# Kernel optimization log

Hardware: AMD Instinct MI355X
Metric: run time of the kernel (lower is better)

## Reference

```python
import jax, jax.numpy as jnp
import numpy as np
from jax import lax

L, H, NUM_CONVS, KSIZE = 8192, 128, 4, 7
EPS = 1e-5


def _pos_encoding(length, dim, dtype):
    pos = jnp.arange(length, dtype=jnp.float32)[:, None]
    i = jnp.arange(dim, dtype=jnp.float32)[None, :]
    angle = pos / jnp.power(10000.0, (2.0 * jnp.floor(i / 2.0)) / dim)
    pe = jnp.where((jnp.arange(dim) % 2 == 0)[None, :], jnp.sin(angle), jnp.cos(angle))
    return pe.astype(dtype)


def _layer_norm(x):
    mu = jnp.mean(x, axis=-1, keepdims=True)
    var = jnp.mean(jnp.square(x - mu), axis=-1, keepdims=True)
    return (x - mu) * lax.rsqrt(var + EPS)


def _conv1d_same(x, w, b):
    # x: [L, H]; w: [H_out, H_in, K]; b: [H_out]. SAME padding over sequence.
    lhs = x.T[None]  # [1, H, L]
    out = lax.conv_general_dilated(lhs, w, window_strides=(1,), padding='SAME',
                                   dimension_numbers=('NCH', 'OIH', 'NCH'))
    return (out[0] + b[:, None]).T  # [L, H]


def setup_inputs() -> dict:
    key = jax.random.key(0)
    ks = jax.random.split(key, 12)
    s = 0.02
    return {
        'x': jax.random.normal(ks[0], (L, H), jnp.float32),
        'conv_w': jax.random.normal(ks[1], (NUM_CONVS, H, H, KSIZE), jnp.float32) * s,
        'conv_b': jax.random.normal(ks[2], (NUM_CONVS, H), jnp.float32) * s,
        'Wq': jax.random.normal(ks[3], (H, H), jnp.float32) * s,
        'bq': jax.random.normal(ks[4], (H,), jnp.float32) * s,
        'Wk': jax.random.normal(ks[5], (H, H), jnp.float32) * s,
        'bk': jax.random.normal(ks[6], (H,), jnp.float32) * s,
        'Wv': jax.random.normal(ks[7], (H, H), jnp.float32) * s,
        'bv': jax.random.normal(ks[8], (H,), jnp.float32) * s,
        'Wff': jax.random.normal(ks[9], (H, H), jnp.float32) * s,
        'bff': jax.random.normal(ks[10], (H,), jnp.float32) * s,
    }


def reference(x, conv_w, conv_b, Wq, bq, Wk, bk, Wv, bv, Wff, bff):
    h = x + _pos_encoding(x.shape[0], x.shape[1], x.dtype)
    # conv stack: LN -> conv -> residual, repeated num_convs times
    for i in range(NUM_CONVS):
        residual = h
        h = _conv1d_same(_layer_norm(h), conv_w[i], conv_b[i]) + residual
    # self-attention (single-head as written in the source)
    residual = h
    n = _layer_norm(h)
    q = n @ Wq.T + bq
    k = n @ Wk.T + bk
    v = n @ Wv.T + bv
    scale = 1.0 / jnp.sqrt(jnp.asarray(H, h.dtype))
    attn = jax.nn.softmax((q @ k.T) * scale, axis=-1)  # [L, L]
    h = attn @ v + residual
    # feed-forward
    residual = h
    h = jax.nn.relu(_layer_norm(h) @ Wff.T + bff) + residual
    return h
```

## Files before the change

### kernel.cpp

```cpp
#include <hip/hip_runtime.h>

#define LL 8192
#define HH 128

typedef __attribute__((ext_vector_type(8))) short short8v;
typedef __attribute__((ext_vector_type(4))) short short4v;
typedef __attribute__((ext_vector_type(4))) float f32x4;
typedef __attribute__((ext_vector_type(16))) float f32x16;

__device__ inline short f2bf(float f) {
    union { float f; unsigned u; } x; x.f = f;
    unsigned r = (x.u + 0x7fffu + ((x.u >> 16) & 1u)) >> 16;
    return (short)r;
}
__device__ inline float bf2f(short s) {
    union { unsigned u; float f; } x; x.u = ((unsigned)(unsigned short)s) << 16;
    return x.f;
}

__device__ inline float fexp2(float x) {
#if defined(__has_builtin)
#if __has_builtin(__builtin_amdgcn_exp2f)
    return __builtin_amdgcn_exp2f(x);
#else
    return __expf(x * 0.6931471805599453f);
#endif
#else
    return __expf(x * 0.6931471805599453f);
#endif
}

__device__ inline unsigned pack_hi16(unsigned hi, unsigned lo) {
#if defined(__has_builtin)
#if __has_builtin(__builtin_amdgcn_perm)
    return __builtin_amdgcn_perm(hi, lo, 0x07060302u);
#endif
#endif
    return (lo >> 16) | (hi & 0xffff0000u);
}

__device__ inline void plane32swap(unsigned& a, unsigned& b) {
#if defined(__has_builtin)
#if __has_builtin(__builtin_amdgcn_permlane32_swap)
    typedef unsigned u2v __attribute__((ext_vector_type(2)));
    u2v r = __builtin_amdgcn_permlane32_swap(a, b, false, false);
    a = r[0]; b = r[1];
    return;
#endif
#endif
    asm volatile("v_permlane32_swap_b32 %0, %1" : "+v"(a), "+v"(b));
}

__device__ inline short* sAp(short* base, int row, int col) {
    int byte = (row << 8) + (col << 1);
    byte ^= (row & 7) << 4;
    return (short*)((char*)base + byte);
}

__device__ inline short8v ln_pack8(const float* rowF, int l15) {
    const float4 a = *(const float4*)&rowF[l15 * 8];
    const float4 b = *(const float4*)&rowF[l15 * 8 + 4];
    float s  = (a.x + a.y) + (a.z + a.w) + (b.x + b.y) + (b.z + b.w);
    float s2 = a.x * a.x + a.y * a.y + a.z * a.z + a.w * a.w
             + b.x * b.x + b.y * b.y + b.z * b.z + b.w * b.w;
#pragma unroll
    for (int off = 1; off <= 8; off <<= 1) {
        s  += __shfl_xor(s,  off, 64);
        s2 += __shfl_xor(s2, off, 64);
    }
    float mu = s * (1.f / 128.f);
    float var = s2 * (1.f / 128.f) - mu * mu;
    float rstd = rsqrtf(var + 1e-5f);
    short8v r;
    r[0] = f2bf((a.x - mu) * rstd);
    r[1] = f2bf((a.y - mu) * rstd);
    r[2] = f2bf((a.z - mu) * rstd);
    r[3] = f2bf((a.w - mu) * rstd);
    r[4] = f2bf((b.x - mu) * rstd);
    r[5] = f2bf((b.y - mu) * rstd);
    r[6] = f2bf((b.z - mu) * rstd);
    r[7] = f2bf((b.w - mu) * rstd);
    return r;
}

__global__ __launch_bounds__(256) void repack_all(const float* __restrict__ x,
                                                  const float* __restrict__ w,
                                                  const float* __restrict__ Wq,
                                                  const float* __restrict__ Wk,
                                                  const float* __restrict__ Wv,
                                                  const float* __restrict__ bq,
                                                  const float* __restrict__ bk,
                                                  const float* __restrict__ bv,
                                                  const float* __restrict__ Wff,
                                                  short* __restrict__ wkb,
                                                  short* __restrict__ wqkvb,
                                                  float* __restrict__ b3,
                                                  short* __restrict__ wffb,
                                                  float* __restrict__ h0) {
    const float qs = 0.08838834764831845f * 1.4426950408889634f;
    int idx = blockIdx.x * 256 + threadIdx.x;
    if (idx < 458752) {
        int k = idx % 7;
        int t = idx / 7;
        int i = t % HH; t /= HH;
        int o = t % HH;
        int lay = t / HH;
        wkb[((lay * 7 + k) * HH + o) * HH + i] = f2bf(w[idx]);
    } else {
        int j = idx - 458752;
        if (j < 49152) {
            int t = j >> 14, r = j & 16383;
            float v = (t == 0) ? Wq[r] * qs : (t == 1) ? Wk[r] : Wv[r];
            wqkvb[j] = f2bf(v);
        } else if (j < 49536) {
            int jj = j - 49152;
            b3[jj] = (jj < 128) ? bq[jj] * qs : (jj < 256) ? bk[jj - 128] : bv[jj - 256];
        } else if (j < 65920) {
            int jj = j - 49536;
            wffb[jj] = f2bf(Wff[jj]);
        } else {
            int p = j - 65920;
            if (p < 262144) {
                int g = p >> 5, c4 = (p & 31) << 2;
                float4 val = *(const float4*)&x[g * HH + c4];
                float fg = (float)g;
#pragma unroll
                for (int h = 0; h < 2; h++) {
                    int i0 = c4 + h * 2;
                    float e = (float)i0 / 128.f;
                    float rev = fg * fexp2(e * -13.287712379549449f - 2.651496129472319f);
                    rev -= floorf(rev);
                    float ang = rev * 6.283185307179586f;
                    ((float*)&val)[h * 2]     += __sinf(ang);
                    ((float*)&val)[h * 2 + 1] += __cosf(ang);
                }
                *(float4*)&h0[g * HH + c4] = val;
            }
        }
    }
}

__global__ __launch_bounds__(256, 2) void conv4_qkv_kernel(const float* __restrict__ h0,
                                                           const short* __restrict__ wkb,
                                                           const float* __restrict__ conv_b,
                                                           const short* __restrict__ wqkvb,
                                                           const float* __restrict__ b3,
                                                           float* __restrict__ hB,
                                                           short* __restrict__ qb,
                                                           short* __restrict__ kb,
                                                           short* __restrict__ vt) {
    __shared__ float sF[40][132];
    __shared__ short sA[54 * 128];
    __shared__ short sT[4][32][17];
    int tid = threadIdx.x;
    int w = tid >> 6, lane = tid & 63;
    int l15 = lane & 15, quad = lane >> 4;
    int wg = blockIdx.x;
    int m0 = ((wg & 7) * 64 + (wg >> 3)) * 16;
    int c0 = w * 32;

    for (int idx = tid; idx < 40 * 32; idx += 256) {
        int r = idx >> 5, c4 = (idx & 31) << 2;
        int g = m0 - 12 + r;
        float4 val = make_float4(0.f, 0.f, 0.f, 0.f);
        if (g >= 0 && g < LL) val = *(const float4*)&h0[g * HH + c4];
        *(float4*)&sF[r][c4] = val;
    }
    __syncthreads();
#pragma unroll
    for (int rr = 0; rr < 3; rr++) {
        int row = rr * 16 + w * 4 + quad;
        if (row < 40)
            *(short8v*)sAp(sA, row, l15 * 8) = ln_pack8(&sF[row][0], l15);
    }
    __syncthreads();

    const float* cb = conv_b;
#define CONV_TILE(wl, B, aca, acb)                                                  \
    {                                                                               \
        for (int k = 0; k < 7; k++) {                                               \
            const short* bw0 = (wl) + (k * HH + c0 + l15) * HH;                     \
            const short* bw1 = bw0 + 16 * HH;                                       \
            _Pragma("unroll")                                                       \
            for (int ks = 0; ks < 4; ks++) {                                        \
                short8v bf0 = *(const short8v*)&bw0[ks * 32 + quad * 8];            \
                short8v bf1 = *(const short8v*)&bw1[ks * 32 + quad * 8];            \
                short8v af = *(const short8v*)sAp(sA, (B) - 3 + l15 + k,            \
                                                  ks * 32 + quad * 8);              \
                aca = __builtin_amdgcn_mfma_f32_16x16x32_bf16(af, bf0, aca, 0, 0, 0); \
                acb = __builtin_amdgcn_mfma_f32_16x16x32_bf16(af, bf1, acb, 0, 0, 0); \
            }                                                                       \
        }                                                                           \
    }

    {
        const short* wl = wkb + 0 * 7 * HH * HH;
        f32x4 a0a = (f32x4)(0.f), a0b = (f32x4)(0.f);
        f32x4 a1a = (f32x4)(0.f), a1b = (f32x4)(0.f);
        f32x4 a2a = (f32x4)(0.f), a2b = (f32x4)(0.f);
        CONV_TILE(wl, 3,  a0a, a0b);
        CONV_TILE(wl, 19, a1a, a1b);
        CONV_TILE(wl, 35, a2a, a2b);
        float bl = cb[0 * HH + c0 + l15], bh = cb[0 * HH + c0 + 16 + l15];
#pragma unroll
        for (int r = 0; r < 4; r++) {
            int rr0 = quad * 4 + r;
            sF[3 + rr0][c0 + l15]       += a0a[r] + bl;
            sF[3 + rr0][c0 + 16 + l15]  += a0b[r] + bh;
            sF[19 + rr0][c0 + l15]      += a1a[r] + bl;
            sF[19 + rr0][c0 + 16 + l15] += a1b[r] + bh;
            if (rr0 < 2) {
                sF[35 + rr0][c0 + l15]      += a2a[r] + bl;
                sF[35 + rr0][c0 + 16 + l15] += a2b[r] + bh;
            }
        }
    }
    __syncthreads();
#pragma unroll
    for (int rr = 0; rr < 3; rr++) {
        int row = 3 + rr * 16 + w * 4 + quad;
        if (row < 37) {
            short8v pk = ln_pack8(&sF[row][0], l15);
            int g = m0 - 12 + row;
            if (g < 0 || g >= LL) pk = (short8v)(short)0;
            *(short8v*)sAp(sA, row, l15 * 8) = pk;
        }
    }
    __syncthreads();

    {
        const short* wl = wkb + 1 * 7 * HH * HH;
        f32x4 a0a = (f32x4)(0.f), a0b = (f32x4)(0.f);
        f32x4 a1a = (f32x4)(0.f), a1b = (f32x4)(0.f);
        CONV_TILE(wl, 6,  a0a, a0b);
        CONV_TILE(wl, 22, a1a, a1b);
        float bl = cb[1 * HH + c0 + l15], bh = cb[1 * HH + c0 + 16 + l15];
#pragma unroll
        for (int r = 0; r < 4; r++) {
            int rr0 = quad * 4 + r;
            sF[6 + rr0][c0 + l15]      += a0a[r] + bl;
            sF[6 + rr0][c0 + 16 + l15] += a0b[r] + bh;
            if (rr0 < 12) {
                sF[22 + rr0][c0 + l15]      += a1a[r] + bl;
                sF[22 + rr0][c0 + 16 + l15] += a1b[r] + bh;
            }
        }
    }
    __syncthreads();
#pragma unroll
    for (int rr = 0; rr < 2; rr++) {
        int row = 6 + rr * 16 + w * 4 + quad;
        if (row < 34) {
            short8v pk = ln_pack8(&sF[row][0], l15);
            int g = m0 - 12 + row;
            if (g < 0 || g >= LL) pk = (short8v)(short)0;
            *(short8v*)sAp(sA, row, l15 * 8) = pk;
        }
    }
    __syncthreads();

    {
        const short* wl = wkb + 2 * 7 * HH * HH;
        f32x4 a0a = (f32x4)(0.f), a0b = (f32x4)(0.f);
        f32x4 a1a = (f32x4)(0.f), a1b = (f32x4)(0.f);
        CONV_TILE(wl, 9,  a0a, a0b);
        CONV_TILE(wl, 25, a1a, a1b);
        float bl = cb[2 * HH + c0 + l15], bh = cb[2 * HH + c0 + 16 + l15];
#pragma unroll
        for (int r = 0; r < 4; r++) {
            int rr0 = quad * 4 + r;
            sF[9 + rr0][c0 + l15]      += a0a[r] + bl;
            sF[9 + rr0][c0 + 16 + l15] += a0b[r] + bh;
            if (rr0 < 6) {
                sF[25 + rr0][c0 + l15]      += a1a[r] + bl;
                sF[25 + rr0][c0 + 16 + l15] += a1b[r] + bh;
            }
        }
    }
    __syncthreads();
#pragma unroll
    for (int rr = 0; rr < 2; rr++) {
        int row = 9 + rr * 16 + w * 4 + quad;
        if (row < 31) {
            short8v pk = ln_pack8(&sF[row][0], l15);
            int g = m0 - 12 + row;
            if (g < 0 || g >= LL) pk = (short8v)(short)0;
            *(short8v*)sAp(sA, row, l15 * 8) = pk;
        }
    }
    __syncthreads();

    {
        const short* wl = wkb + 3 * 7 * HH * HH;
        f32x4 a0a = (f32x4)(0.f), a0b = (f32x4)(0.f);
        CONV_TILE(wl, 12, a0a, a0b);
        float bl = cb[3 * HH + c0 + l15], bh = cb[3 * HH + c0 + 16 + l15];
#pragma unroll
        for (int r = 0; r < 4; r++) {
            int rr0 = quad * 4 + r;
            int g = m0 + rr0;
            float v0 = sF[12 + rr0][c0 + l15]      + a0a[r] + bl;
            float v1 = sF[12 + rr0][c0 + 16 + l15] + a0b[r] + bh;
            sF[12 + rr0][c0 + l15]      = v0;
            sF[12 + rr0][c0 + 16 + l15] = v1;
            hB[g * HH + c0 + l15]      = v0;
            hB[g * HH + c0 + 16 + l15] = v1;
        }
    }
    __syncthreads();
#undef CONV_TILE
    {
        int row = w * 4 + quad;
        *(short8v*)sAp(sA, row, l15 * 8) = ln_pack8(&sF[12 + row][0], l15);
    }
    __syncthreads();
    short8v af4[4];
#pragma unroll
    for (int ks = 0; ks < 4; ks++)
        af4[ks] = *(const short8v*)sAp(sA, l15, ks * 32 + quad * 8);

    for (int t = 0; t < 3; t++) {
        f32x4 acc0 = (f32x4)(0.f), acc1 = (f32x4)(0.f);
        const short* b0 = wqkvb + (t * 128 + c0 + l15) * HH;
        const short* b1 = b0 + 16 * HH;
#pragma unroll
        for (int ks = 0; ks < 4; ks++) {
            short8v bf0 = *(const short8v*)&b0[ks * 32 + quad * 8];
            short8v bf1 = *(const short8v*)&b1[ks * 32 + quad * 8];
            acc0 = __builtin_amdgcn_mfma_f32_16x16x32_bf16(af4[ks], bf0, acc0, 0, 0, 0);
            acc1 = __builtin_amdgcn_mfma_f32_16x16x32_bf16(af4[ks], bf1, acc1, 0, 0, 0);
        }
        float qb0 = b3[t * 128 + c0 + l15], qb1 = b3[t * 128 + c0 + 16 + l15];
        if (t < 2) {
            short* o = (t == 0) ? qb : kb;
#pragma unroll
            for (int r = 0; r < 4; r++) {
                int lr = m0 + quad * 4 + r;
                o[lr * HH + c0 + l15]      = f2bf(acc0[r] + qb0);
                o[lr * HH + c0 + 16 + l15] = f2bf(acc1[r] + qb1);
            }
        } else {
#pragma unroll
            for (int r = 0; r < 4; r++) {
                sT[w][l15][quad * 4 + r]      = f2bf(acc0[r] + qb0);
                sT[w][16 + l15][quad * 4 + r] = f2bf(acc1[r] + qb1);
            }
            asm volatile("s_waitcnt lgkmcnt(0)" ::: "memory");
#pragma unroll
            for (int cc = 0; cc < 8; cc++) {
                int col = cc * 4 + quad;
                vt[(c0 + col) * LL + m0 + l15] = sT[w][col][l15];
            }
        }
    }
}

#define FBN 64
#define NSPLIT 8
#define SEGROWS (LL / NSPLIT)

__global__ __launch_bounds__(256, 2) void flash_mfma_kernel(const short* __restrict__ qs,
                                                            const short* __restrict__ ksrc,
                                                            const short* __restrict__ vsrc,
                                                            short* __restrict__ PO,
                                                            float* __restrict__ Pl) {
    __shared__ short sK[16 * 64 * 8];
    __shared__ short sV[16 * 64 * 8];

    const int tid = threadIdx.x;
    const int w = tid >> 6, lane = tid & 63;
    const int l31 = lane & 31, hi = lane >> 5;
    const int seg = blockIdx.x & 7;
    const int m0 = (blockIdx.x >> 3) * 128;
    const int jbeg = seg * SEGROWS;
    const int nchunk = SEGROWS >> 6;
    const int qrow = m0 + w * 32 + l31;

    short8v qf[8];
#pragma unroll
    for (int ks = 0; ks < 8; ks++)
        qf[ks] = *(const short8v*)&qs[qrow * HH + ks * 16 + hi * 8];

    float l_r = 0.f;
    f32x16 o_acc[4];
#pragma unroll
    for (int dt = 0; dt < 4; dt++) o_acc[dt] = (f32x16)(0.f);

    short8v kr[4], vr[4];
#pragma unroll
    for (int r = 0; r < 4; r++) {
        int s = w + 4 * r;
        kr[r] = *(const short8v*)&ksrc[(jbeg + (s >> 3) * 32 + l31) * HH + (s & 7) * 16 + hi * 8];
        vr[r] = *(const short8v*)&vsrc[((s >> 2) * 32 + l31) * LL + jbeg + (s & 3) * 16 + hi * 8];
    }

    for (int c = 0; c < nchunk; c++) {
        __syncthreads();
#pragma unroll
        for (int r = 0; r < 4; r++) {
            int s = w + 4 * r;
            *(short8v*)&sK[(s * 64 + lane) * 8] = kr[r];
            *(short8v*)&sV[(s * 64 + lane) * 8] = vr[r];
        }
        __syncthreads();
        if (c + 1 < nchunk) {
            const int j1 = jbeg + (c + 1) * FBN;
#pragma unroll
            for (int r = 0; r < 4; r++) {
                int s = w + 4 * r;
                kr[r] = *(const short8v*)&ksrc[(j1 + (s >> 3) * 32 + l31) * HH + (s & 7) * 16 + hi * 8];
                vr[r] = *(const short8v*)&vsrc[((s >> 2) * 32 + l31) * LL + j1 + (s & 3) * 16 + hi * 8];
            }
        }
        f32x16 s0 = (f32x16)(0.f), s1 = (f32x16)(0.f);
        __builtin_amdgcn_s_setprio(1);
#pragma unroll
        for (int ks = 0; ks < 8; ks++) {
            short8v kf0 = *(const short8v*)&sK[((ks) * 64 + lane) * 8];
            short8v kf1 = *(const short8v*)&sK[((8 + ks) * 64 + lane) * 8];
            s0 = __builtin_amdgcn_mfma_f32_32x32x16_bf16(kf0, qf[ks], s0, 0, 0, 0);
            s1 = __builtin_amdgcn_mfma_f32_32x32x16_bf16(kf1, qf[ks], s1, 0, 0, 0);
        }
        __builtin_amdgcn_s_setprio(0);
        short8v pfrag[4];
#pragma unroll
        for (int nt = 0; nt < 2; nt++) {
            const f32x16& sa = nt ? s1 : s0;
            unsigned pw[8];
#pragma unroll
            for (int m = 0; m < 8; m++) {
                float p0 = fexp2(sa[2 * m]);
                float p1 = fexp2(sa[2 * m + 1]);
                l_r += p0 + p1;
                union { float f; unsigned u; } u0, u1;
                u0.f = p0; u1.f = p1;
                pw[m] = pack_hi16(u1.u, u0.u);
            }
            plane32swap(pw[0], pw[2]);
            plane32swap(pw[1], pw[3]);
            plane32swap(pw[4], pw[6]);
            plane32swap(pw[5], pw[7]);
            union { unsigned u[4]; short8v v; } fa, fb;
            fa.u[0] = pw[0]; fa.u[1] = pw[1]; fa.u[2] = pw[2]; fa.u[3] = pw[3];
            fb.u[0] = pw[4]; fb.u[1] = pw[5]; fb.u[2] = pw[6]; fb.u[3] = pw[7];
            pfrag[nt * 2]     = fa.v;
            pfrag[nt * 2 + 1] = fb.v;
        }
        __builtin_amdgcn_s_setprio(1);
#pragma unroll
        for (int ks = 0; ks < 4; ks++)
#pragma unroll
            for (int dt = 0; dt < 4; dt++) {
                short8v vf = *(const short8v*)&sV[((dt * 4 + ks) * 64 + lane) * 8];
                o_acc[dt] = __builtin_amdgcn_mfma_f32_32x32x16_bf16(pfrag[ks], vf, o_acc[dt], 0, 0, 0);
            }
        __builtin_amdgcn_s_setprio(0);
    }
    float lsum = l_r + __shfl_xor(l_r, 32, 64);
    if (hi == 0)
        Pl[seg * LL + qrow] = lsum;
#pragma unroll
    for (int dt = 0; dt < 4; dt++)
#pragma unroll
        for (int i = 0; i < 16; i++) {
            int qr = (i & 3) + 8 * (i >> 2) + 4 * hi;
            PO[(size_t)seg * LL * HH + (size_t)(m0 + w * 32 + qr) * HH + dt * 32 + l31] =
                f2bf(o_acc[dt][i]);
        }
}

__global__ __launch_bounds__(256) void ff_kernel(const float* __restrict__ hin,
                                                 const short* __restrict__ PO,
                                                 const float* __restrict__ Pl,
                                                 const short* __restrict__ wffb,
                                                 const float* __restrict__ bff,
                                                 float* __restrict__ out) {
    __shared__ float sF[16][132];
    __shared__ short sA[16 * 128];
    __shared__ float sLi[16];
    int tid = threadIdx.x;
    int w = tid >> 6, lane = tid & 63;
    int l15 = lane & 15, quad = lane >> 4;
    int wg = blockIdx.x;
    int m0 = ((wg & 7) * 64 + (wg >> 3)) * 16;

    if (tid < 16) {
        float s = 0.f;
#pragma unroll
        for (int seg = 0; seg < NSPLIT; seg++) s += Pl[seg * LL + m0 + tid];
        sLi[tid] = 1.f / s;
    }
    __syncthreads();
    for (int idx = tid; idx < 16 * 32; idx += 256) {
        int r = idx >> 5, c4 = (idx & 31) << 2;
        float4 hv = *(const float4*)&hin[(m0 + r) * HH + c4];
        float s0 = 0.f, s1 = 0.f, s2 = 0.f, s3 = 0.f;
#pragma unroll
        for (int seg = 0; seg < NSPLIT; seg++) {
            short4v pv = *(const short4v*)&PO[(size_t)seg * LL * HH + (m0 + r) * HH + c4];
            s0 += bf2f(pv[0]); s1 += bf2f(pv[1]); s2 += bf2f(pv[2]); s3 += bf2f(pv[3]);
        }
        float li = sLi[r];
        *(float4*)&sF[r][c4] = make_float4(hv.x + s0 * li, hv.y + s1 * li,
                                           hv.z + s2 * li, hv.w + s3 * li);
    }
    __syncthreads();
    {
        int row = w * 4 + quad;
        *(short8v*)sAp(sA, row, l15 * 8) = ln_pack8(&sF[row][0], l15);
    }
    __syncthreads();
    int c0 = w * 32;
    f32x4 acc0 = (f32x4)(0.f), acc1 = (f32x4)(0.f);
    const short* b0 = wffb + (c0 + l15) * HH;
    const short* b1 = b0 + 16 * HH;
#pragma unroll
    for (int ks = 0; ks < 4; ks++) {
        short8v af = *(const short8v*)sAp(sA, l15, ks * 32 + quad * 8);
        short8v bf0 = *(const short8v*)&b0[ks * 32 + quad * 8];
        short8v bf1 = *(const short8v*)&b1[ks * 32 + quad * 8];
        acc0 = __builtin_amdgcn_mfma_f32_16x16x32_bf16(af, bf0, acc0, 0, 0, 0);
        acc1 = __builtin_amdgcn_mfma_f32_16x16x32_bf16(af, bf1, acc1, 0, 0, 0);
    }
    float bb0 = bff[c0 + l15], bb1 = bff[c0 + 16 + l15];
#pragma unroll
    for (int r = 0; r < 4; r++) {
        int lr = quad * 4 + r;
        out[(m0 + lr) * HH + c0 + l15]      = fmaxf(acc0[r] + bb0, 0.f) + sF[lr][c0 + l15];
        out[(m0 + lr) * HH + c0 + 16 + l15] = fmaxf(acc1[r] + bb1, 0.f) + sF[lr][c0 + 16 + l15];
    }
}

extern "C" void kernel_launch(void* const* d_in, const int* in_sizes, int n_in,
                              void* d_out, int out_size, void* d_ws, size_t ws_size,
                              hipStream_t stream) {
    const float* x      = (const float*)d_in[0];
    const float* conv_w = (const float*)d_in[1];
    const float* conv_b = (const float*)d_in[2];
    const float* Wq = (const float*)d_in[3];
    const float* bq = (const float*)d_in[4];
    const float* Wk = (const float*)d_in[5];
    const float* bk = (const float*)d_in[6];
    const float* Wv = (const float*)d_in[7];
    const float* bv = (const float*)d_in[8];
    const float* Wff = (const float*)d_in[9];
    const float* bff = (const float*)d_in[10];
    float* out = (float*)d_out;

    char* ws = (char*)d_ws;
    const size_t MB = 1u << 20;
    float* hB   = (float*)(ws);
    short* qb   = (short*)(ws + 4 * MB);
    short* kb   = (short*)(ws + 6 * MB);
    short* vt   = (short*)(ws + 8 * MB);
    float* Pl   = (float*)(ws + 10 * MB);
    short* wffb = (short*)(ws + 10 * MB + 524288);
    short* PO   = (short*)(ws + 10 * MB + 524288 + 32768);
    short* wkb   = (short*)(ws + 16 * MB);
    short* wqkvb = (short*)(ws + 17 * MB);
    float* b3    = (float*)(ws + 17 * MB + 131072);
    float* h0    = (float*)(ws + 18 * MB);

    repack_all<<<3074, 256, 0, stream>>>(x, conv_w, Wq, Wk, Wv, bq, bk, bv, Wff,
                                         wkb, wqkvb, b3, wffb, h0);
    conv4_qkv_kernel<<<LL / 16, 256, 0, stream>>>(h0, wkb, conv_b, wqkvb, b3,
                                                  hB, qb, kb, vt);
    flash_mfma_kernel<<<LL / 128 * NSPLIT, 256, 0, stream>>>(qb, kb, vt, PO, Pl);
    ff_kernel<<<LL / 16, 256, 0, stream>>>(hB, PO, Pl, wffb, bff, out);
}
```

Before: 195.0 us.

## Split conv/QKV kernel across eight waves with 16 output columns each

Doubles the conv4_qkv block size from 256 to 512 threads so each of eight waves owns 16 output columns instead of 32. Each wave's MFMA work is split across two accumulators by alternating k-slices, which keeps two independent dependency chains. Layer-norm packing is redone with a helper that stores two 4-element halves. The aim is more parallelism and latency hiding in the conv stage. The cost is extra per-wave LDS A-fragment reads, since A is now loaded per 16 columns, and heavier register pressure under launch bounds of 4 blocks of 512.

```diff
diff --git a/kernel.cpp b/kernel.cpp
--- a/kernel.cpp
+++ b/kernel.cpp
@@ -81,6 +81,30 @@
     r[6] = f2bf((b.z - mu) * rstd);
     r[7] = f2bf((b.w - mu) * rstd);
     return r;
+}
+
+__device__ inline void ln_store8(const float* rowF, int l15, short* sA, int row, bool zero) {
+    const float4 a = *(const float4*)&rowF[l15 * 4];
+    const float4 b = *(const float4*)&rowF[64 + l15 * 4];
+    float s  = (a.x + a.y) + (a.z + a.w) + (b.x + b.y) + (b.z + b.w);
+    float s2 = a.x * a.x + a.y * a.y + a.z * a.z + a.w * a.w
+             + b.x * b.x + b.y * b.y + b.z * b.z + b.w * b.w;
+#pragma unroll
+    for (int off = 1; off <= 8; off <<= 1) {
+        s  += __shfl_xor(s,  off, 64);
+        s2 += __shfl_xor(s2, off, 64);
+    }
+    float mu = s * (1.f / 128.f);
+    float var = s2 * (1.f / 128.f) - mu * mu;
+    float rstd = rsqrtf(var + 1e-5f);
+    short4v ra, rb;
+    ra[0] = f2bf((a.x - mu) * rstd); ra[1] = f2bf((a.y - mu) * rstd);
+    ra[2] = f2bf((a.z - mu) * rstd); ra[3] = f2bf((a.w - mu) * rstd);
+    rb[0] = f2bf((b.x - mu) * rstd); rb[1] = f2bf((b.y - mu) * rstd);
+    rb[2] = f2bf((b.z - mu) * rstd); rb[3] = f2bf((b.w - mu) * rstd);
+    if (zero) { ra = (short4v)(short)0; rb = (short4v)(short)0; }
+    *(short4v*)sAp(sA, row, l15 * 4)      = ra;
+    *(short4v*)sAp(sA, row, 64 + l15 * 4) = rb;
 }
 
 __global__ __launch_bounds__(256) void repack_all(const float* __restrict__ x,
@@ -140,7 +164,7 @@
     }
 }
 
-__global__ __launch_bounds__(256, 2) void conv4_qkv_kernel(const float* __restrict__ h0,
+__global__ __launch_bounds__(512, 4) void conv4_qkv_kernel(const float* __restrict__ h0,
                                                            const short* __restrict__ wkb,
                                                            const float* __restrict__ conv_b,
                                                            const short* __restrict__ wqkvb,
@@ -151,15 +175,15 @@
                                                            short* __restrict__ vt) {
     __shared__ float sF[40][132];
     __shared__ short sA[54 * 128];
-    __shared__ short sT[4][32][17];
+    __shared__ short sT[8][16][17];
     int tid = threadIdx.x;
     int w = tid >> 6, lane = tid & 63;
     int l15 = lane & 15, quad = lane >> 4;
     int wg = blockIdx.x;
     int m0 = ((wg & 7) * 64 + (wg >> 3)) * 16;
-    int c0 = w * 32;
-
-    for (int idx = tid; idx < 40 * 32; idx += 256) {
+    int c0w = w * 16;
+
+    for (int idx = tid; idx < 40 * 32; idx += 512) {
         int r = idx >> 5, c4 = (idx & 31) << 2;
         int g = m0 - 12 + r;
         float4 val = make_float4(0.f, 0.f, 0.f, 0.f);
@@ -168,150 +192,128 @@
     }
     __syncthreads();
 #pragma unroll
-    for (int rr = 0; rr < 3; rr++) {
-        int row = rr * 16 + w * 4 + quad;
+    for (int rr = 0; rr < 2; rr++) {
+        int row = rr * 32 + w * 4 + quad;
         if (row < 40)
-            *(short8v*)sAp(sA, row, l15 * 8) = ln_pack8(&sF[row][0], l15);
+            ln_store8(&sF[row][0], l15, sA, row, false);
     }
     __syncthreads();
 
     const float* cb = conv_b;
-#define CONV_TILE(wl, B, aca, acb)                                                  \
+#define CONV_TILE(wl, B, acA, acB)                                                  \
     {                                                                               \
         for (int k = 0; k < 7; k++) {                                               \
-            const short* bw0 = (wl) + (k * HH + c0 + l15) * HH;                     \
-            const short* bw1 = bw0 + 16 * HH;                                       \
+            const short* bw = (wl) + (k * HH + c0w + l15) * HH;                     \
             _Pragma("unroll")                                                       \
             for (int ks = 0; ks < 4; ks++) {                                        \
-                short8v bf0 = *(const short8v*)&bw0[ks * 32 + quad * 8];            \
-                short8v bf1 = *(const short8v*)&bw1[ks * 32 + quad * 8];            \
+                short8v bf = *(const short8v*)&bw[ks * 32 + quad * 8];              \
                 short8v af = *(const short8v*)sAp(sA, (B) - 3 + l15 + k,            \
                                                   ks * 32 + quad * 8);              \
-                aca = __builtin_amdgcn_mfma_f32_16x16x32_bf16(af, bf0, aca, 0, 0, 0); \
-                acb = __builtin_amdgcn_mfma_f32_16x16x32_bf16(af, bf1, acb, 0, 0, 0); \
+                if (ks & 1) acB = __builtin_amdgcn_mfma_f32_16x16x32_bf16(af, bf, acB, 0, 0, 0); \
+                else        acA = __builtin_amdgcn_mfma_f32_16x16x32_bf16(af, bf, acA, 0, 0, 0); \
             }                                                                       \
         }                                                                           \
     }
 
     {
         const short* wl = wkb + 0 * 7 * HH * HH;
-        f32x4 a0a = (f32x4)(0.f), a0b = (f32x4)(0.f);
-        f32x4 a1a = (f32x4)(0.f), a1b = (f32x4)(0.f);
-        f32x4 a2a = (f32x4)(0.f), a2b = (f32x4)(0.f);
-        CONV_TILE(wl, 3,  a0a, a0b);
-        CONV_TILE(wl, 19, a1a, a1b);
-        CONV_TILE(wl, 35, a2a, a2b);
-        float bl = cb[0 * HH + c0 + l15], bh = cb[0 * HH + c0 + 16 + l15];
+        f32x4 a0A = (f32x4)(0.f), a0B = (f32x4)(0.f);
+        f32x4 a1A = (f32x4)(0.f), a1B = (f32x4)(0.f);
+        f32x4 a2A = (f32x4)(0.f), a2B = (f32x4)(0.f);
+        CONV_TILE(wl, 3,  a0A, a0B);
+        CONV_TILE(wl, 19, a1A, a1B);
+        CONV_TILE(wl, 35, a2A, a2B);
+        float bb = cb[0 * HH + c0w + l15];
 #pragma unroll
         for (int r = 0; r < 4; r++) {
             int rr0 = quad * 4 + r;
-            sF[3 + rr0][c0 + l15]       += a0a[r] + bl;
-            sF[3 + rr0][c0 + 16 + l15]  += a0b[r] + bh;
-            sF[19 + rr0][c0 + l15]      += a1a[r] + bl;
-            sF[19 + rr0][c0 + 16 + l15] += a1b[r] + bh;
-            if (rr0 < 2) {
-                sF[35 + rr0][c0 + l15]      += a2a[r] + bl;
-                sF[35 + rr0][c0 + 16 + l15] += a2b[r] + bh;
-            }
-        }
-    }
-    __syncthreads();
-#pragma unroll
-    for (int rr = 0; rr < 3; rr++) {
-        int row = 3 + rr * 16 + w * 4 + quad;
+            sF[3 + rr0][c0w + l15]  += a0A[r] + a0B[r] + bb;
+            sF[19 + rr0][c0w + l15] += a1A[r] + a1B[r] + bb;
+            if (rr0 < 2)
+                sF[35 + rr0][c0w + l15] += a2A[r] + a2B[r] + bb;
+        }
+    }
+    __syncthreads();
+#pragma unroll
+    for (int rr = 0; rr < 2; rr++) {
+        int row = 3 + rr * 32 + w * 4 + quad;
         if (row < 37) {
-            short8v pk = ln_pack8(&sF[row][0], l15);
             int g = m0 - 12 + row;
-            if (g < 0 || g >= LL) pk = (short8v)(short)0;
-            *(short8v*)sAp(sA, row, l15 * 8) = pk;
+            ln_store8(&sF[row][0], l15, sA, row, (g < 0 || g >= LL));
         }
     }
     __syncthreads();
 
     {
         const short* wl = wkb + 1 * 7 * HH * HH;
-        f32x4 a0a = (f32x4)(0.f), a0b = (f32x4)(0.f);
-        f32x4 a1a = (f32x4)(0.f), a1b = (f32x4)(0.f);
-        CONV_TILE(wl, 6,  a0a, a0b);
-        CONV_TILE(wl, 22, a1a, a1b);
-        float bl = cb[1 * HH + c0 + l15], bh = cb[1 * HH + c0 + 16 + l15];
+        f32x4 a0A = (f32x4)(0.f), a0B = (f32x4)(0.f);
+        f32x4 a1A = (f32x4)(0.f), a1B = (f32x4)(0.f);
+        CONV_TILE(wl, 6,  a0A, a0B);
+        CONV_TILE(wl, 22, a1A, a1B);
+        float bb = cb[1 * HH + c0w + l15];
 #pragma unroll
         for (int r = 0; r < 4; r++) {
             int rr0 = quad * 4 + r;
-            sF[6 + rr0][c0 + l15]      += a0a[r] + bl;
-            sF[6 + rr0][c0 + 16 + l15] += a0b[r] + bh;
-            if (rr0 < 12) {
-                sF[22 + rr0][c0 + l15]      += a1a[r] + bl;
-                sF[22 + rr0][c0 + 16 + l15] += a1b[r] + bh;
-            }
-        }
-    }
-    __syncthreads();
-#pragma unroll
-    for (int rr = 0; rr < 2; rr++) {
-        int row = 6 + rr * 16 + w * 4 + quad;
+            sF[6 + rr0][c0w + l15] += a0A[r] + a0B[r] + bb;
+            if (rr0 < 12)
+                sF[22 + rr0][c0w + l15] += a1A[r] + a1B[r] + bb;
+        }
+    }
+    __syncthreads();
+    {
+        int row = 6 + w * 4 + quad;
         if (row < 34) {
-            short8v pk = ln_pack8(&sF[row][0], l15);
             int g = m0 - 12 + row;
-            if (g < 0 || g >= LL) pk = (short8v)(short)0;
-            *(short8v*)sAp(sA, row, l15 * 8) = pk;
+            ln_store8(&sF[row][0], l15, sA, row, (g < 0 || g >= LL));
         }
     }
     __syncthreads();
 
     {
         const short* wl = wkb + 2 * 7 * HH * HH;
-        f32x4 a0a = (f32x4)(0.f), a0b = (f32x4)(0.f);
-        f32x4 a1a = (f32x4)(0.f), a1b = (f32x4)(0.f);
-        CONV_TILE(wl, 9,  a0a, a0b);
-        CONV_TILE(wl, 25, a1a, a1b);
-        float bl = cb[2 * HH + c0 + l15], bh = cb[2 * HH + c0 + 16 + l15];
+        f32x4 a0A = (f32x4)(0.f), a0B = (f32x4)(0.f);
+        f32x4 a1A = (f32x4)(0.f), a1B = (f32x4)(0.f);
+        CONV_TILE(wl, 9,  a0A, a0B);
+        CONV_TILE(wl, 25, a1A, a1B);
+        float bb = cb[2 * HH + c0w + l15];
 #pragma unroll
         for (int r = 0; r < 4; r++) {
             int rr0 = quad * 4 + r;
-            sF[9 + rr0][c0 + l15]      += a0a[r] + bl;
-            sF[9 + rr0][c0 + 16 + l15] += a0b[r] + bh;
-            if (rr0 < 6) {
-                sF[25 + rr0][c0 + l15]      += a1a[r] + bl;
-                sF[25 + rr0][c0 + 16 + l15] += a1b[r] + bh;
-            }
-        }
-    }
-    __syncthreads();
-#pragma unroll
-    for (int rr = 0; rr < 2; rr++) {
-        int row = 9 + rr * 16 + w * 4 + quad;
+            sF[9 + rr0][c0w + l15] += a0A[r] + a0B[r] + bb;
+            if (rr0 < 6)
+                sF[25 + rr0][c0w + l15] += a1A[r] + a1B[r] + bb;
+        }
+    }
+    __syncthreads();
+    {
+        int row = 9 + w * 4 + quad;
         if (row < 31) {
-            short8v pk = ln_pack8(&sF[row][0], l15);
             int g = m0 - 12 + row;
-            if (g < 0 || g >= LL) pk = (short8v)(short)0;
-            *(short8v*)sAp(sA, row, l15 * 8) = pk;
+            ln_store8(&sF[row][0], l15, sA, row, (g < 0 || g >= LL));
         }
     }
     __syncthreads();
 
     {
         const short* wl = wkb + 3 * 7 * HH * HH;
-        f32x4 a0a = (f32x4)(0.f), a0b = (f32x4)(0.f);
-        CONV_TILE(wl, 12, a0a, a0b);
-        float bl = cb[3 * HH + c0 + l15], bh = cb[3 * HH + c0 + 16 + l15];
+        f32x4 aA = (f32x4)(0.f), aB = (f32x4)(0.f);
+        CONV_TILE(wl, 12, aA, aB);
+        float bb = cb[3 * HH + c0w + l15];
 #pragma unroll
         for (int r = 0; r < 4; r++) {
             int rr0 = quad * 4 + r;
             int g = m0 + rr0;
-            float v0 = sF[12 + rr0][c0 + l15]      + a0a[r] + bl;
-            float v1 = sF[12 + rr0][c0 + 16 + l15] + a0b[r] + bh;
-            sF[12 + rr0][c0 + l15]      = v0;
-            sF[12 + rr0][c0 + 16 + l15] = v1;
-            hB[g * HH + c0 + l15]      = v0;
-            hB[g * HH + c0 + 16 + l15] = v1;
+            float v0 = sF[12 + rr0][c0w + l15] + aA[r] + aB[r] + bb;
+            sF[12 + rr0][c0w + l15] = v0;
+            hB[g * HH + c0w + l15] = v0;
         }
     }
     __syncthreads();
 #undef CONV_TILE
     {
         int row = w * 4 + quad;
-        *(short8v*)sAp(sA, row, l15 * 8) = ln_pack8(&sF[12 + row][0], l15);
+        if (row < 16)
+            ln_store8(&sF[12 + row][0], l15, sA, row, false);
     }
     __syncthreads();
     short8v af4[4];
@@ -320,36 +322,31 @@
         af4[ks] = *(const short8v*)sAp(sA, l15, ks * 32 + quad * 8);
 
     for (int t = 0; t < 3; t++) {
-        f32x4 acc0 = (f32x4)(0.f), acc1 = (f32x4)(0.f);
-        const short* b0 = wqkvb + (t * 128 + c0 + l15) * HH;
-        const short* b1 = b0 + 16 * HH;
+        f32x4 acA = (f32x4)(0.f), acB = (f32x4)(0.f);
+        const short* b0 = wqkvb + (t * 128 + c0w + l15) * HH;
 #pragma unroll
         for (int ks = 0; ks < 4; ks++) {
-            short8v bf0 = *(const short8v*)&b0[ks * 32 + quad * 8];
-            short8v bf1 = *(const short8v*)&b1[ks * 32 + quad * 8];
-            acc0 = __builtin_amdgcn_mfma_f32_16x16x32_bf16(af4[ks], bf0, acc0, 0, 0, 0);
-            acc1 = __builtin_amdgcn_mfma_f32_16x16x32_bf16(af4[ks], bf1, acc1, 0, 0, 0);
-        }
-        float qb0 = b3[t * 128 + c0 + l15], qb1 = b3[t * 128 + c0 + 16 + l15];
+            short8v bf = *(const short8v*)&b0[ks * 32 + quad * 8];
+            if (ks & 1) acB = __builtin_amdgcn_mfma_f32_16x16x32_bf16(af4[ks], bf, acB, 0, 0, 0);
+            else        acA = __builtin_amdgcn_mfma_f32_16x16x32_bf16(af4[ks], bf, acA, 0, 0, 0);
+        }
+        float qb0 = b3[t * 128 + c0w + l15];
         if (t < 2) {
             short* o = (t == 0) ? qb : kb;
 #pragma unroll
             for (int r = 0; r < 4; r++) {
                 int lr = m0 + quad * 4 + r;
-                o[lr * HH + c0 + l15]      = f2bf(acc0[r] + qb0);
-                o[lr * HH + c0 + 16 + l15] = f2bf(acc1[r] + qb1);
+                o[lr * HH + c0w + l15] = f2bf(acA[r] + acB[r] + qb0);
             }
         } else {
 #pragma unroll
-            for (int r = 0; r < 4; r++) {
-                sT[w][l15][quad * 4 + r]      = f2bf(acc0[r] + qb0);
-                sT[w][16 + l15][quad * 4 + r] = f2bf(acc1[r] + qb1);
-            }
+            for (int r = 0; r < 4; r++)
+                sT[w][l15][quad * 4 + r] = f2bf(acA[r] + acB[r] + qb0);
             asm volatile("s_waitcnt lgkmcnt(0)" ::: "memory");
 #pragma unroll
-            for (int cc = 0; cc < 8; cc++) {
+            for (int cc = 0; cc < 4; cc++) {
                 int col = cc * 4 + quad;
-                vt[(c0 + col) * LL + m0 + l15] = sT[w][col][l15];
+                vt[(c0w + col) * LL + m0 + l15] = sT[w][col][l15];
             }
         }
     }
@@ -563,7 +560,7 @@
 
     repack_all<<<3074, 256, 0, stream>>>(x, conv_w, Wq, Wk, Wv, bq, bk, bv, Wff,
                                          wkb, wqkvb, b3, wffb, h0);
-    conv4_qkv_kernel<<<LL / 16, 256, 0, stream>>>(h0, wkb, conv_b, wqkvb, b3,
+    conv4_qkv_kernel<<<LL / 16, 512, 0, stream>>>(h0, wkb, conv_b, wqkvb, b3,
                                                   hB, qb, kb, vt);
     flash_mfma_kernel<<<LL / 128 * NSPLIT, 256, 0, stream>>>(qb, kb, vt, PO, Pl);
     ff_kernel<<<LL / 16, 256, 0, stream>>>(hB, PO, Pl, wffb, bff, out);
```

After: 195.3 us. About the same (+0.1%).
